# Kernel optimization log

Hardware: AMD Instinct MI355X
Metric: run time of the kernel (lower is better)

## Reference

```python
import jax, jax.numpy as jnp
import numpy as np

B, C_IN, H, W = 16, 128, 224, 224
C_OUT, KH, KW = 256, 3, 3
STRIDE = (2, 3)
PAD = 1


def setup_inputs() -> dict:
    key = jax.random.key(0)
    kx, kw, kb = jax.random.split(key, 3)
    x = jax.random.normal(kx, (B, C_IN, H, W), dtype=jnp.float32)
    weight = jax.random.normal(kw, (C_OUT, C_IN, KH, KW), dtype=jnp.float32)
    bias = jax.random.normal(kb, (C_OUT,), dtype=jnp.float32)
    return {"x": x, "weight": weight, "bias": bias}


def reference(x, weight, bias):
    # Faithful conv2d: zero-pad by 1 on each side, stride (2,3), kernel 3x3,
    # per-output-channel dot product + bias (same math as the quadruple-loop torch code).
    out = jax.lax.conv_general_dilated(
        x, weight,
        window_strides=STRIDE,
        padding=[(PAD, PAD), (PAD, PAD)],
        dimension_numbers=("NCHW", "OIHW", "NCHW"),
    )
    return out + bias[None, :, None, None]
```

## Files before the change

### kernel.cpp

```cpp
#include <hip/hip_runtime.h>
#include <cstdint>

constexpr int B_   = 16;
constexpr int CIN  = 128;
constexpr int H_   = 224;
constexpr int W_   = 224;
constexpr int COUT = 256;
constexpr int HOUT = 112;
constexpr int WOUT = 75;

constexpr int CI_SC = 16;
constexpr int KSC_R = 144;
constexpr int KP    = 160;
constexpr int NSC   = 8;
constexpr int THREADS = 256;

constexpr int WS_SH8  = COUT * KP * NSC / 8;
constexpr size_t WS_NEED = (size_t)WS_SH8 * 16;

constexpr int B_OFF   = 25600;
constexpr int LDS_TOT = B_OFF + 3 * 16384;

typedef float  f32x4   __attribute__((ext_vector_type(4)));
typedef short  short8  __attribute__((ext_vector_type(8)));
typedef unsigned int uint32x4 __attribute__((ext_vector_type(4)));

struct U64x2 { unsigned long long lo, hi; };
__device__ inline short8 bc8(unsigned long long a, unsigned long long b) {
  U64x2 u{a, b};
  return __builtin_bit_cast(short8, u);
}
__device__ inline short8 cv8(uint32x4 v) { return __builtin_bit_cast(short8, v); }

__device__ inline unsigned cvtpk(float a, float b) {
  unsigned r;
  asm("v_cvt_pk_bf16_f32 %0, %1, %2" : "=v"(r) : "v"(a), "v"(b));
  return r;
}

__device__ __forceinline__ void gload_lds(const void* g, void* l) {
  __builtin_amdgcn_global_load_lds((const __attribute__((address_space(1))) void*)g,
                                   (__attribute__((address_space(3))) void*)l, 16, 0, 0);
}

__global__ __launch_bounds__(256) void wprep(const float* __restrict__ wgt,
                                             uint4* __restrict__ ws) {
  int o  = blockIdx.x * 256 + threadIdx.x;
  int co = o & 255;
  int t  = o >> 8;
  int g  = t & 3;
  int u  = t >> 2;
  int kc = u % 5;
  int sc = u / 5;
  int kloc = kc * 32 + g * 8;
  float f[8];
  if (kloc < KSC_R) {
    const float* p = wgt + (size_t)co * 1152 + sc * KSC_R + kloc;
    float4 a = *(const float4*)p;
    float4 b = *(const float4*)(p + 4);
    f[0] = a.x; f[1] = a.y; f[2] = a.z; f[3] = a.w;
    f[4] = b.x; f[5] = b.y; f[6] = b.z; f[7] = b.w;
  } else {
#pragma unroll
    for (int e = 0; e < 8; ++e) f[e] = 0.f;
  }
  ws[o] = uint4{cvtpk(f[0], f[1]), cvtpk(f[2], f[3]), cvtpk(f[4], f[5]), cvtpk(f[6], f[7])};
}

__device__ __forceinline__ short8 load_bq(const float* q, int kc, int g) {
  if (kc == 4 && g >= 2) return short8{};
  const float* s = q + kc * 32;
  float4 x0 = *(const float4*)s, x1 = *(const float4*)(s + 4);
  uint4 u{cvtpk(x0.x, x0.y), cvtpk(x0.z, x0.w), cvtpk(x1.x, x1.y), cvtpk(x1.z, x1.w)};
  return __builtin_bit_cast(short8, u);
}

#define TR_ISSUE(S, KC)                                                                   \
  {                                                                                       \
    unsigned a_ = abase + (unsigned)((KC) * 5120);                                        \
    asm volatile("ds_read_b64_tr_b16 %0, %1"             : "=v"(S##0) : "v"(a_));         \
    asm volatile("ds_read_b64_tr_b16 %0, %1 offset:640"  : "=v"(S##1) : "v"(a_));         \
    asm volatile("ds_read_b64_tr_b16 %0, %1 offset:128"  : "=v"(S##2) : "v"(a_));         \
    asm volatile("ds_read_b64_tr_b16 %0, %1 offset:768"  : "=v"(S##3) : "v"(a_));         \
    asm volatile("ds_read_b64_tr_b16 %0, %1 offset:256"  : "=v"(S##4) : "v"(a_));         \
    asm volatile("ds_read_b64_tr_b16 %0, %1 offset:896"  : "=v"(S##5) : "v"(a_));         \
    asm volatile("ds_read_b64_tr_b16 %0, %1 offset:384"  : "=v"(S##6) : "v"(a_));         \
    asm volatile("ds_read_b64_tr_b16 %0, %1 offset:1024" : "=v"(S##7) : "v"(a_));         \
    asm volatile("ds_read_b64_tr_b16 %0, %1 offset:512"  : "=v"(S##8) : "v"(a_));         \
    asm volatile("ds_read_b64_tr_b16 %0, %1 offset:1152" : "=v"(S##9) : "v"(a_));         \
  }

#define B_ISSUE(BR, BB)                                                                   \
  asm volatile("ds_read_b128 %0, %1"             : "=v"(BR##0) : "v"(BB));                \
  asm volatile("ds_read_b128 %0, %1 offset:1024" : "=v"(BR##1) : "v"(BB));                \
  asm volatile("ds_read_b128 %0, %1 offset:2048" : "=v"(BR##2) : "v"(BB));                \
  asm volatile("ds_read_b128 %0, %1 offset:3072" : "=v"(BR##3) : "v"(BB));

#define B_DMA(GT, BS)                                                                     \
  {                                                                                       \
    const char* s_ = wsl + (size_t)(GT) * 16384;                                          \
    char* d_ = bD + (BS) * 16384;                                                         \
    gload_lds(s_,       d_);                                                              \
    gload_lds(s_ + 256, d_ + 1024);                                                       \
    gload_lds(s_ + 512, d_ + 2048);                                                       \
    gload_lds(s_ + 768, d_ + 3072);                                                       \
  }

#define VMGATE(N)                                                                         \
  asm volatile("s_waitcnt vmcnt(" #N ")" ::: "memory");                                   \
  __builtin_amdgcn_sched_barrier(0);

#define WAITLG(N)                                                                         \
  asm volatile("s_waitcnt lgkmcnt(" #N ")" ::: "memory");                                 \
  __builtin_amdgcn_sched_barrier(0);

#define MFMA_SET(S, B0, B1, B2, B3)                                                       \
  {                                                                                       \
    short8 a0_ = bc8(S##0, S##1);                                                         \
    short8 a1_ = bc8(S##2, S##3);                                                         \
    short8 a2_ = bc8(S##4, S##5);                                                         \
    short8 a3_ = bc8(S##6, S##7);                                                         \
    short8 a4_ = bc8(S##8, S##9);                                                         \
    __builtin_amdgcn_s_setprio(1);                                                        \
    acc[0][0] = __builtin_amdgcn_mfma_f32_16x16x32_bf16(a0_, B0, acc[0][0], 0, 0, 0);     \
    acc[0][1] = __builtin_amdgcn_mfma_f32_16x16x32_bf16(a0_, B1, acc[0][1], 0, 0, 0);     \
    acc[0][2] = __builtin_amdgcn_mfma_f32_16x16x32_bf16(a0_, B2, acc[0][2], 0, 0, 0);     \
    acc[0][3] = __builtin_amdgcn_mfma_f32_16x16x32_bf16(a0_, B3, acc[0][3], 0, 0, 0);     \
    acc[1][0] = __builtin_amdgcn_mfma_f32_16x16x32_bf16(a1_, B0, acc[1][0], 0, 0, 0);     \
    acc[1][1] = __builtin_amdgcn_mfma_f32_16x16x32_bf16(a1_, B1, acc[1][1], 0, 0, 0);     \
    acc[1][2] = __builtin_amdgcn_mfma_f32_16x16x32_bf16(a1_, B2, acc[1][2], 0, 0, 0);     \
    acc[1][3] = __builtin_amdgcn_mfma_f32_16x16x32_bf16(a1_, B3, acc[1][3], 0, 0, 0);     \
    acc[2][0] = __builtin_amdgcn_mfma_f32_16x16x32_bf16(a2_, B0, acc[2][0], 0, 0, 0);     \
    acc[2][1] = __builtin_amdgcn_mfma_f32_16x16x32_bf16(a2_, B1, acc[2][1], 0, 0, 0);     \
    acc[2][2] = __builtin_amdgcn_mfma_f32_16x16x32_bf16(a2_, B2, acc[2][2], 0, 0, 0);     \
    acc[2][3] = __builtin_amdgcn_mfma_f32_16x16x32_bf16(a2_, B3, acc[2][3], 0, 0, 0);     \
    acc[3][0] = __builtin_amdgcn_mfma_f32_16x16x32_bf16(a3_, B0, acc[3][0], 0, 0, 0);     \
    acc[3][1] = __builtin_amdgcn_mfma_f32_16x16x32_bf16(a3_, B1, acc[3][1], 0, 0, 0);     \
    acc[3][2] = __builtin_amdgcn_mfma_f32_16x16x32_bf16(a3_, B2, acc[3][2], 0, 0, 0);     \
    acc[3][3] = __builtin_amdgcn_mfma_f32_16x16x32_bf16(a3_, B3, acc[3][3], 0, 0, 0);     \
    acc[4][0] = __builtin_amdgcn_mfma_f32_16x16x32_bf16(a4_, B0, acc[4][0], 0, 0, 0);     \
    acc[4][1] = __builtin_amdgcn_mfma_f32_16x16x32_bf16(a4_, B1, acc[4][1], 0, 0, 0);     \
    acc[4][2] = __builtin_amdgcn_mfma_f32_16x16x32_bf16(a4_, B2, acc[4][2], 0, 0, 0);     \
    acc[4][3] = __builtin_amdgcn_mfma_f32_16x16x32_bf16(a4_, B3, acc[4][3], 0, 0, 0);     \
    __builtin_amdgcn_s_setprio(0);                                                        \
  }

template <int WS>
__global__ __launch_bounds__(THREADS, 2) void conv_mfma(
    const float* __restrict__ x, const float* __restrict__ wgt,
    const short8* __restrict__ wbf, const float* __restrict__ bias,
    float* __restrict__ out) {

  __shared__ __align__(16) unsigned char smem[LDS_TOT];

  int Lid = (blockIdx.x & 7) * 224 + (blockIdx.x >> 3);
  int oh  = Lid % 112;
  int b   = Lid / 112;

  const int tid   = threadIdx.x;
  const int lane  = tid & 63;
  const int cogrp = tid >> 6;
  const int g     = lane >> 4;
  const int l15   = lane & 15;

  const float* xb = x + (size_t)b * CIN * H_ * W_;
  const int coB_  = cogrp * 64 + l15;

  const unsigned sbase = (unsigned)(uintptr_t)&smem[0];
  const unsigned abase = sbase + (unsigned)(g * 1280 + l15 * 8);
  const unsigned vB    = sbase + (unsigned)(B_OFF + cogrp * 4096 + lane * 16);
  char* bD = (char*)&smem[B_OFF + cogrp * 4096];
  const char* wsl = (const char*)wbf + (size_t)(g * 4096 + cogrp * 1024 + l15 * 16);

  if (tid < 160) {
    *reinterpret_cast<uint4*>(&smem[23040 + tid * 16]) = uint4{0u, 0u, 0u, 0u};
  }

  f32x4 acc[5][4];
#pragma unroll
  for (int mf = 0; mf < 5; ++mf)
#pragma unroll
    for (int cf = 0; cf < 4; ++cf)
#pragma unroll
      for (int i = 0; i < 4; ++i) acc[mf][cf][i] = 0.f;

  unsigned long long tA0, tA1, tA2, tA3, tA4, tA5, tA6, tA7, tA8, tA9;
  unsigned long long tB0, tB1, tB2, tB3, tB4, tB5, tB6, tB7, tB8, tB9;
  uint32x4 brA0, brA1, brA2, brA3, brB0, brB1, brB2, brB3;

  int bsel = 0, gkc = 0, gt;
  unsigned bb;
  if (WS) { B_DMA(0, 0) B_DMA(1, 1) B_DMA(2, 2) }

  for (int sc = 0; sc < NSC; ++sc) {
    if (sc) __syncthreads();

    const float* xs = xb + (size_t)sc * (CI_SC * H_ * W_);
#pragma unroll
    for (int j = 0; j < 4; ++j) {
      int it = tid + THREADS * j;
      if (j < 3 || it < 912) {
        int gg  = it % 19;
        int rid = it / 19;
        int ci  = rid & 15;
        int kh  = rid >> 4;
        int ih  = 2 * oh - 1 + kh;
        bool rowok = (unsigned)ih < (unsigned)H_;
        int ro  = (ci * H_ + (rowok ? ih : 0)) * W_;
        int iwb = 12 * gg;
        unsigned mAj = rowok ? 0xFFFFFFFFu : 0u;
        unsigned mFj = mAj & (gg ? 0xFFFFFFFFu : 0xFFFF0000u);

        const float* ap = xs + (ro + iwb);
        float4 a4 = *(const float4*)ap;
        float4 b4 = *(const float4*)(ap + 4);
        float4 c4 = *(const float4*)(xs + (ro + (iwb + 8 > 220 ? 220 : iwb + 8)));
        float fm1 = xs[ro + iwb - (gg ? 1 : 0)];

        int k = ci * 9 + kh * 3;
        int m = 4 * gg;
        unsigned base = (unsigned)(((k >> 2) * 5 + (m >> 4)) * 128 + (m & 15) * 2);
        unsigned o0 = base + (unsigned)((k & 3) * 32);
        unsigned o1 = base + (unsigned)(((k + 1) & 3) * 32) + (((k + 1) >> 2) - (k >> 2)) * 640u;
        unsigned o2 = base + (unsigned)(((k + 2) & 3) * 32) + (((k + 2) >> 2) - (k >> 2)) * 640u;

        unsigned l0 = cvtpk(fm1,  a4.z) & mFj;
        unsigned h0 = cvtpk(b4.y, c4.x) & mAj;
        unsigned l1 = cvtpk(a4.x, a4.w) & mAj;
        unsigned h1 = cvtpk(b4.z, c4.y) & mAj;
        unsigned l2 = cvtpk(a4.y, b4.x) & mAj;
        unsigned h2 = cvtpk(b4.w, c4.z) & mAj;
        *(uint2*)&smem[o0] = make_uint2(l0, h0);
        *(uint2*)&smem[o1] = make_uint2(l1, h1);
        *(uint2*)&smem[o2] = make_uint2(l2, h2);
      }
    }
    __syncthreads();

    if (WS) {
      const int b1 = bsel + 1 == 3 ? 0 : bsel + 1;
      const int b2 = b1 + 1 == 3 ? 0 : b1 + 1;

      VMGATE(8);
      bb = vB + (unsigned)bsel * 16384u;
      B_ISSUE(brA, bb);
      TR_ISSUE(tA, 0);

      VMGATE(4);
      bb = vB + (unsigned)b1 * 16384u;
      B_ISSUE(brB, bb);
      TR_ISSUE(tB, 1);
      WAITLG(14);
      { short8 c0 = cv8(brA0), c1 = cv8(brA1), c2 = cv8(brA2), c3 = cv8(brA3);
        MFMA_SET(tA, c0, c1, c2, c3); }
      gt = gkc + 3; if (gt > 39) gt = 39;
      B_DMA(gt, bsel);
      ++gkc;

      VMGATE(4);
      bb = vB + (unsigned)b2 * 16384u;
      B_ISSUE(brA, bb);
      TR_ISSUE(tA, 2);
      WAITLG(14);
      { short8 c0 = cv8(brB0), c1 = cv8(brB1), c2 = cv8(brB2), c3 = cv8(brB3);
        MFMA_SET(tB, c0, c1, c2, c3); }
      gt = gkc + 3; if (gt > 39) gt = 39;
      B_DMA(gt, b1);
      ++gkc;

      VMGATE(4);
      bb = vB + (unsigned)bsel * 16384u;
      B_ISSUE(brB, bb);
      TR_ISSUE(tB, 3);
      WAITLG(14);
      { short8 c0 = cv8(brA0), c1 = cv8(brA1), c2 = cv8(brA2), c3 = cv8(brA3);
        MFMA_SET(tA, c0, c1, c2, c3); }
      gt = gkc + 3; if (gt > 39) gt = 39;
      B_DMA(gt, b2);
      ++gkc;

      VMGATE(4);
      bb = vB + (unsigned)b1 * 16384u;
      B_ISSUE(brA, bb);
      TR_ISSUE(tA, 4);
      WAITLG(14);
      { short8 c0 = cv8(brB0), c1 = cv8(brB1), c2 = cv8(brB2), c3 = cv8(brB3);
        MFMA_SET(tB, c0, c1, c2, c3); }
      gt = gkc + 3; if (gt > 39) gt = 39;
      B_DMA(gt, bsel);
      ++gkc;

      WAITLG(0);
      { short8 c0 = cv8(brA0), c1 = cv8(brA1), c2 = cv8(brA2), c3 = cv8(brA3);
        MFMA_SET(tA, c0, c1, c2, c3); }
      gt = gkc + 3; if (gt > 39) gt = 39;
      B_DMA(gt, b1);
      ++gkc;

      bsel = b2;
    } else {
      const float* q0 = wgt + (size_t)coB_ * 1152 + sc * 144 + g * 8;
      const float* q1 = q0 + (size_t)16 * 1152;
      const float* q2 = q0 + (size_t)32 * 1152;
      const float* q3 = q0 + (size_t)48 * 1152;
#pragma unroll
      for (int kc = 0; kc < 5; ++kc) {
        short8 c0 = load_bq(q0, kc, g), c1 = load_bq(q1, kc, g);
        short8 c2 = load_bq(q2, kc, g), c3 = load_bq(q3, kc, g);
        TR_ISSUE(tA, kc);
        WAITLG(0);
        MFMA_SET(tA, c0, c1, c2, c3);
      }
    }
  }

  asm volatile("s_waitcnt vmcnt(0)" ::: "memory");

  float bv0 = bias[coB_];
  float bv1 = bias[coB_ + 16];
  float bv2 = bias[coB_ + 32];
  float bv3 = bias[coB_ + 48];
  size_t ob0 = (((size_t)b * COUT + coB_) * HOUT + oh) * WOUT;
  size_t ob1 = ob0 + (size_t)16 * HOUT * WOUT;
  size_t ob2 = ob0 + (size_t)32 * HOUT * WOUT;
  size_t ob3 = ob0 + (size_t)48 * HOUT * WOUT;
#pragma unroll
  for (int mf = 0; mf < 5; ++mf) {
    int owb = mf * 16 + g * 4;
#pragma unroll
    for (int r = 0; r < 4; ++r) {
      int ow = owb + r;
      if (ow < WOUT) {
        out[ob0 + ow] = acc[mf][0][r] + bv0;
        out[ob1 + ow] = acc[mf][1][r] + bv1;
        out[ob2 + ow] = acc[mf][2][r] + bv2;
        out[ob3 + ow] = acc[mf][3][r] + bv3;
      }
    }
  }
}

extern "C" void kernel_launch(void* const* d_in, const int* in_sizes, int n_in,
                              void* d_out, int out_size, void* d_ws, size_t ws_size,
                              hipStream_t stream) {
  const float* x    = (const float*)d_in[0];
  const float* wgt  = (const float*)d_in[1];
  const float* bias = (const float*)d_in[2];
  float* out        = (float*)d_out;

  dim3 grid(16 * 112);
  dim3 block(THREADS);

  if (ws_size >= WS_NEED) {
    wprep<<<dim3(WS_SH8 / 256), dim3(256), 0, stream>>>(wgt, (uint4*)d_ws);
    conv_mfma<1><<<grid, block, 0, stream>>>(x, wgt, (const short8*)d_ws, bias, out);
  } else {
    conv_mfma<0><<<grid, block, 0, stream>>>(x, wgt, (const short8*)d_ws, bias, out);
  }
}
```

Before: 200.0 us.

## Split output channels across two blocks to raise occupancy

Each block now computes 128 output channels instead of 256, so each wave handles 32 channels with half the accumulators. The grid doubles and launch bounds rise to 3 blocks per CU, and the LDS weight ring buffer shrinks to match. The aim is more concurrent waves for latency hiding, at the cost of gathering and converting the input tile twice, since im2col work is repeated per channel half.

```diff
diff --git a/kernel.cpp b/kernel.cpp
--- a/kernel.cpp
+++ b/kernel.cpp
@@ -19,7 +19,7 @@
 constexpr size_t WS_NEED = (size_t)WS_SH8 * 16;
 
 constexpr int B_OFF   = 25600;
-constexpr int LDS_TOT = B_OFF + 3 * 16384;
+constexpr int LDS_TOT = B_OFF + 4 * 3 * 2048;
 
 typedef float  f32x4   __attribute__((ext_vector_type(4)));
 typedef short  short8  __attribute__((ext_vector_type(8)));
@@ -92,18 +92,14 @@
 
 #define B_ISSUE(BR, BB)                                                                   \
   asm volatile("ds_read_b128 %0, %1"             : "=v"(BR##0) : "v"(BB));                \
-  asm volatile("ds_read_b128 %0, %1 offset:1024" : "=v"(BR##1) : "v"(BB));                \
-  asm volatile("ds_read_b128 %0, %1 offset:2048" : "=v"(BR##2) : "v"(BB));                \
-  asm volatile("ds_read_b128 %0, %1 offset:3072" : "=v"(BR##3) : "v"(BB));
+  asm volatile("ds_read_b128 %0, %1 offset:1024" : "=v"(BR##1) : "v"(BB));
 
 #define B_DMA(GT, BS)                                                                     \
   {                                                                                       \
     const char* s_ = wsl + (size_t)(GT) * 16384;                                          \
-    char* d_ = bD + (BS) * 16384;                                                         \
+    char* d_ = bD + (BS) * 2048;                                                          \
     gload_lds(s_,       d_);                                                              \
     gload_lds(s_ + 256, d_ + 1024);                                                       \
-    gload_lds(s_ + 512, d_ + 2048);                                                       \
-    gload_lds(s_ + 768, d_ + 3072);                                                       \
   }
 
 #define VMGATE(N)                                                                         \
@@ -114,7 +110,7 @@
   asm volatile("s_waitcnt lgkmcnt(" #N ")" ::: "memory");                                 \
   __builtin_amdgcn_sched_barrier(0);
 
-#define MFMA_SET(S, B0, B1, B2, B3)                                                       \
+#define MFMA_SET(S, B0, B1)                                                               \
   {                                                                                       \
     short8 a0_ = bc8(S##0, S##1);                                                         \
     short8 a1_ = bc8(S##2, S##3);                                                         \
@@ -124,38 +120,30 @@
     __builtin_amdgcn_s_setprio(1);                                                        \
     acc[0][0] = __builtin_amdgcn_mfma_f32_16x16x32_bf16(a0_, B0, acc[0][0], 0, 0, 0);     \
     acc[0][1] = __builtin_amdgcn_mfma_f32_16x16x32_bf16(a0_, B1, acc[0][1], 0, 0, 0);     \
-    acc[0][2] = __builtin_amdgcn_mfma_f32_16x16x32_bf16(a0_, B2, acc[0][2], 0, 0, 0);     \
-    acc[0][3] = __builtin_amdgcn_mfma_f32_16x16x32_bf16(a0_, B3, acc[0][3], 0, 0, 0);     \
     acc[1][0] = __builtin_amdgcn_mfma_f32_16x16x32_bf16(a1_, B0, acc[1][0], 0, 0, 0);     \
     acc[1][1] = __builtin_amdgcn_mfma_f32_16x16x32_bf16(a1_, B1, acc[1][1], 0, 0, 0);     \
-    acc[1][2] = __builtin_amdgcn_mfma_f32_16x16x32_bf16(a1_, B2, acc[1][2], 0, 0, 0);     \
-    acc[1][3] = __builtin_amdgcn_mfma_f32_16x16x32_bf16(a1_, B3, acc[1][3], 0, 0, 0);     \
     acc[2][0] = __builtin_amdgcn_mfma_f32_16x16x32_bf16(a2_, B0, acc[2][0], 0, 0, 0);     \
     acc[2][1] = __builtin_amdgcn_mfma_f32_16x16x32_bf16(a2_, B1, acc[2][1], 0, 0, 0);     \
-    acc[2][2] = __builtin_amdgcn_mfma_f32_16x16x32_bf16(a2_, B2, acc[2][2], 0, 0, 0);     \
-    acc[2][3] = __builtin_amdgcn_mfma_f32_16x16x32_bf16(a2_, B3, acc[2][3], 0, 0, 0);     \
     acc[3][0] = __builtin_amdgcn_mfma_f32_16x16x32_bf16(a3_, B0, acc[3][0], 0, 0, 0);     \
     acc[3][1] = __builtin_amdgcn_mfma_f32_16x16x32_bf16(a3_, B1, acc[3][1], 0, 0, 0);     \
-    acc[3][2] = __builtin_amdgcn_mfma_f32_16x16x32_bf16(a3_, B2, acc[3][2], 0, 0, 0);     \
-    acc[3][3] = __builtin_amdgcn_mfma_f32_16x16x32_bf16(a3_, B3, acc[3][3], 0, 0, 0);     \
     acc[4][0] = __builtin_amdgcn_mfma_f32_16x16x32_bf16(a4_, B0, acc[4][0], 0, 0, 0);     \
     acc[4][1] = __builtin_amdgcn_mfma_f32_16x16x32_bf16(a4_, B1, acc[4][1], 0, 0, 0);     \
-    acc[4][2] = __builtin_amdgcn_mfma_f32_16x16x32_bf16(a4_, B2, acc[4][2], 0, 0, 0);     \
-    acc[4][3] = __builtin_amdgcn_mfma_f32_16x16x32_bf16(a4_, B3, acc[4][3], 0, 0, 0);     \
     __builtin_amdgcn_s_setprio(0);                                                        \
   }
 
 template <int WS>
-__global__ __launch_bounds__(THREADS, 2) void conv_mfma(
+__global__ __launch_bounds__(THREADS, 3) void conv_mfma(
     const float* __restrict__ x, const float* __restrict__ wgt,
     const short8* __restrict__ wbf, const float* __restrict__ bias,
     float* __restrict__ out) {
 
   __shared__ __align__(16) unsigned char smem[LDS_TOT];
 
-  int Lid = (blockIdx.x & 7) * 224 + (blockIdx.x >> 3);
-  int oh  = Lid % 112;
-  int b   = Lid / 112;
+  int Lid   = (blockIdx.x & 7) * 448 + (blockIdx.x >> 3);
+  int coBlk = Lid & 1;
+  int t     = Lid >> 1;
+  int oh    = t % 112;
+  int b     = t / 112;
 
   const int tid   = threadIdx.x;
   const int lane  = tid & 63;
@@ -164,29 +152,30 @@
   const int l15   = lane & 15;
 
   const float* xb = x + (size_t)b * CIN * H_ * W_;
-  const int coB_  = cogrp * 64 + l15;
+  const int coB_  = coBlk * 128 + cogrp * 32 + l15;
 
   const unsigned sbase = (unsigned)(uintptr_t)&smem[0];
   const unsigned abase = sbase + (unsigned)(g * 1280 + l15 * 8);
-  const unsigned vB    = sbase + (unsigned)(B_OFF + cogrp * 4096 + lane * 16);
-  char* bD = (char*)&smem[B_OFF + cogrp * 4096];
-  const char* wsl = (const char*)wbf + (size_t)(g * 4096 + cogrp * 1024 + l15 * 16);
+  const unsigned vB    = sbase + (unsigned)(B_OFF + cogrp * 6144 + lane * 16);
+  char* bD = (char*)&smem[B_OFF + cogrp * 6144];
+  const char* wsl = (const char*)wbf +
+      (size_t)(g * 4096 + (coBlk * 128 + cogrp * 32 + l15) * 16);
 
   if (tid < 160) {
     *reinterpret_cast<uint4*>(&smem[23040 + tid * 16]) = uint4{0u, 0u, 0u, 0u};
   }
 
-  f32x4 acc[5][4];
+  f32x4 acc[5][2];
 #pragma unroll
   for (int mf = 0; mf < 5; ++mf)
 #pragma unroll
-    for (int cf = 0; cf < 4; ++cf)
+    for (int cf = 0; cf < 2; ++cf)
 #pragma unroll
       for (int i = 0; i < 4; ++i) acc[mf][cf][i] = 0.f;
 
   unsigned long long tA0, tA1, tA2, tA3, tA4, tA5, tA6, tA7, tA8, tA9;
   unsigned long long tB0, tB1, tB2, tB3, tB4, tB5, tB6, tB7, tB8, tB9;
-  uint32x4 brA0, brA1, brA2, brA3, brB0, brB1, brB2, brB3;
+  uint32x4 brA0, brA1, brB0, brB1;
 
   int bsel = 0, gkc = 0, gt;
   unsigned bb;
@@ -241,58 +230,58 @@
       const int b1 = bsel + 1 == 3 ? 0 : bsel + 1;
       const int b2 = b1 + 1 == 3 ? 0 : b1 + 1;
 
-      VMGATE(8);
-      bb = vB + (unsigned)bsel * 16384u;
+      VMGATE(4);
+      bb = vB + (unsigned)bsel * 2048u;
       B_ISSUE(brA, bb);
       TR_ISSUE(tA, 0);
 
-      VMGATE(4);
-      bb = vB + (unsigned)b1 * 16384u;
+      VMGATE(2);
+      bb = vB + (unsigned)b1 * 2048u;
       B_ISSUE(brB, bb);
       TR_ISSUE(tB, 1);
-      WAITLG(14);
-      { short8 c0 = cv8(brA0), c1 = cv8(brA1), c2 = cv8(brA2), c3 = cv8(brA3);
-        MFMA_SET(tA, c0, c1, c2, c3); }
+      WAITLG(12);
+      { short8 c0 = cv8(brA0), c1 = cv8(brA1);
+        MFMA_SET(tA, c0, c1); }
       gt = gkc + 3; if (gt > 39) gt = 39;
       B_DMA(gt, bsel);
       ++gkc;
 
-      VMGATE(4);
-      bb = vB + (unsigned)b2 * 16384u;
+      VMGATE(2);
+      bb = vB + (unsigned)b2 * 2048u;
       B_ISSUE(brA, bb);
       TR_ISSUE(tA, 2);
-      WAITLG(14);
-      { short8 c0 = cv8(brB0), c1 = cv8(brB1), c2 = cv8(brB2), c3 = cv8(brB3);
-        MFMA_SET(tB, c0, c1, c2, c3); }
+      WAITLG(12);
+      { short8 c0 = cv8(brB0), c1 = cv8(brB1);
+        MFMA_SET(tB, c0, c1); }
       gt = gkc + 3; if (gt > 39) gt = 39;
       B_DMA(gt, b1);
       ++gkc;
 
-      VMGATE(4);
-      bb = vB + (unsigned)bsel * 16384u;
+      VMGATE(2);
+      bb = vB + (unsigned)bsel * 2048u;
       B_ISSUE(brB, bb);
       TR_ISSUE(tB, 3);
-      WAITLG(14);
-      { short8 c0 = cv8(brA0), c1 = cv8(brA1), c2 = cv8(brA2), c3 = cv8(brA3);
-        MFMA_SET(tA, c0, c1, c2, c3); }
+      WAITLG(12);
+      { short8 c0 = cv8(brA0), c1 = cv8(brA1);
+        MFMA_SET(tA, c0, c1); }
       gt = gkc + 3; if (gt > 39) gt = 39;
       B_DMA(gt, b2);
       ++gkc;
 
-      VMGATE(4);
-      bb = vB + (unsigned)b1 * 16384u;
+      VMGATE(2);
+      bb = vB + (unsigned)b1 * 2048u;
       B_ISSUE(brA, bb);
       TR_ISSUE(tA, 4);
-      WAITLG(14);
-      { short8 c0 = cv8(brB0), c1 = cv8(brB1), c2 = cv8(brB2), c3 = cv8(brB3);
-        MFMA_SET(tB, c0, c1, c2, c3); }
+      WAITLG(12);
+      { short8 c0 = cv8(brB0), c1 = cv8(brB1);
+        MFMA_SET(tB, c0, c1); }
       gt = gkc + 3; if (gt > 39) gt = 39;
       B_DMA(gt, bsel);
       ++gkc;
 
       WAITLG(0);
-      { short8 c0 = cv8(brA0), c1 = cv8(brA1), c2 = cv8(brA2), c3 = cv8(brA3);
-        MFMA_SET(tA, c0, c1, c2, c3); }
+      { short8 c0 = cv8(brA0), c1 = cv8(brA1);
+        MFMA_SET(tA, c0, c1); }
       gt = gkc + 3; if (gt > 39) gt = 39;
       B_DMA(gt, b1);
       ++gkc;
@@ -301,15 +290,12 @@
     } else {
       const float* q0 = wgt + (size_t)coB_ * 1152 + sc * 144 + g * 8;
       const float* q1 = q0 + (size_t)16 * 1152;
-      const float* q2 = q0 + (size_t)32 * 1152;
-      const float* q3 = q0 + (size_t)48 * 1152;
 #pragma unroll
       for (int kc = 0; kc < 5; ++kc) {
         short8 c0 = load_bq(q0, kc, g), c1 = load_bq(q1, kc, g);
-        short8 c2 = load_bq(q2, kc, g), c3 = load_bq(q3, kc, g);
         TR_ISSUE(tA, kc);
         WAITLG(0);
-        MFMA_SET(tA, c0, c1, c2, c3);
+        MFMA_SET(tA, c0, c1);
       }
     }
   }
@@ -318,12 +304,8 @@
 
   float bv0 = bias[coB_];
   float bv1 = bias[coB_ + 16];
-  float bv2 = bias[coB_ + 32];
-  float bv3 = bias[coB_ + 48];
   size_t ob0 = (((size_t)b * COUT + coB_) * HOUT + oh) * WOUT;
   size_t ob1 = ob0 + (size_t)16 * HOUT * WOUT;
-  size_t ob2 = ob0 + (size_t)32 * HOUT * WOUT;
-  size_t ob3 = ob0 + (size_t)48 * HOUT * WOUT;
 #pragma unroll
   for (int mf = 0; mf < 5; ++mf) {
     int owb = mf * 16 + g * 4;
@@ -333,8 +315,6 @@
       if (ow < WOUT) {
         out[ob0 + ow] = acc[mf][0][r] + bv0;
         out[ob1 + ow] = acc[mf][1][r] + bv1;
-        out[ob2 + ow] = acc[mf][2][r] + bv2;
-        out[ob3 + ow] = acc[mf][3][r] + bv3;
       }
     }
   }
@@ -348,7 +328,7 @@
   const float* bias = (const float*)d_in[2];
   float* out        = (float*)d_out;
 
-  dim3 grid(16 * 112);
+  dim3 grid(16 * 112 * 2);
   dim3 block(THREADS);
 
   if (ws_size >= WS_NEED) {
```

Result: slower. 234.3 us (+17.2%).
